# Performance work log

Measured on AMD Instinct MI355X. Metric: run time of the kernel, lower is better.

Reference implementation:

```python
import jax, jax.numpy as jnp
import numpy as np

NUM_NET = 2
V = 100000
D = 128
B = 4096
K = 5
NS = 10
HYP1 = 0.1
HYP2 = 0.1
HYP3 = 0.1


def setup_inputs() -> dict:
    key = jax.random.key(0)
    ks = jax.random.split(key, 10)
    ri = lambda k, shape: jax.random.randint(k, shape, 0, V, dtype=jnp.int32)
    return {
        "node_tables": jax.random.normal(ks[0], (NUM_NET, V, D), jnp.float32) * 0.1,
        "neigh_tables": jax.random.normal(ks[1], (NUM_NET, V, D), jnp.float32) * 0.1,
        "nodes_idx": ri(ks[2], (NUM_NET, B)),
        "neigh_idx": ri(ks[3], (NUM_NET, B, K)),
        "role_idx": ri(ks[4], (NUM_NET, NUM_NET, B)),
        "neg_main": ri(ks[5], (NUM_NET, B, K * NS)),
        "neg_node": ri(ks[6], (NUM_NET, NUM_NET, B, 1 * NS)),
        "neg_cross": ri(ks[7], (NUM_NET, NUM_NET, B, K * NS)),
        "neg_role": ri(ks[8], (NUM_NET, NUM_NET, B, 1 * NS)),
    }


def _pos_loss(ctx, node):
    # ctx: (B, M, D), node: (B, D) -> mean over all logsigmoid(ctx . node)
    return jax.nn.log_sigmoid(jnp.einsum("bmd,bd->bm", ctx, node)).mean()


def _neg_loss(neg_ctx, node):
    # ctx embeddings are negated: logsigmoid(-(neg . node)), sum over samples, mean over batch
    return jax.nn.log_sigmoid(-jnp.einsum("bmd,bd->bm", neg_ctx, node)).sum(axis=1).mean()


def reference(node_tables, neigh_tables, nodes_idx, neigh_idx, role_idx,
              neg_main, neg_node, neg_cross, neg_role):
    cost = []
    for i in range(NUM_NET):
        node_emb = node_tables[i][nodes_idx[i]]          # (B, D)
        # main SGNS loss on view i (neigh tables)
        neigh_emb = neigh_tables[i][neigh_idx[i]]        # (B, K, D)
        c = _pos_loss(neigh_emb, node_emb) + _neg_loss(neigh_tables[i][neg_main[i]], node_emb)
        cost.append(c)
        # cross-view node alignment (node tables of j at same node indices)
        for j in range(NUM_NET):
            if j != i:
                ctx = node_tables[j][nodes_idx[i]][:, None, :]   # (B, 1, D)
                c = _pos_loss(ctx, node_emb) + _neg_loss(node_tables[j][neg_node[i, j]], node_emb)
                cost.append(HYP1 * c)
        # cross-view neighbor loss (neigh tables of j at view-i neighbor indices)
        for j in range(NUM_NET):
            if j != i:
                ctx = neigh_tables[j][neigh_idx[i]]              # (B, K, D)
                c = _pos_loss(ctx, node_emb) + _neg_loss(neigh_tables[j][neg_cross[i, j]], node_emb)
                cost.append(HYP2 * c)
        # role-based loss (node tables of all j at role indices)
        for j in range(NUM_NET):
            ctx = node_tables[j][role_idx[i, j]][:, None, :]     # (B, 1, D)
            c = _pos_loss(ctx, node_emb) + _neg_loss(node_tables[j][neg_role[i, j]], node_emb)
            cost.append(HYP3 * c)
    total = cost[0]
    for c in cost[1:]:
        total = total + c
    return -total / len(cost)
```

## Files before the change

### kernel.cpp

```cpp
#include <hip/hip_runtime.h>

#define NUM_NET 2
#define V 100000
#define D 128
#define B 4096
#define K 5
#define NS 10

#define W_MAIN_POS (1.0f/20480.0f)
#define W_INV_B    (1.0f/4096.0f)
#define HYP_B      (0.1f/4096.0f)
#define HYP2_BK    (0.1f/20480.0f)

#define NBINS 64

__global__ __launch_bounds__(256) void rmne_main(
    const float* __restrict__ node_tables,
    const float* __restrict__ neigh_tables,
    const int*   __restrict__ nodes_idx,
    const int*   __restrict__ neigh_idx,
    const int*   __restrict__ role_idx,
    const int*   __restrict__ neg_main,
    const int*   __restrict__ neg_node,
    const int*   __restrict__ neg_cross,
    const int*   __restrict__ neg_role,
    float*       __restrict__ ws)
{
    const int tid  = threadIdx.x;
    const int lane = tid & 63;
    const int wave = tid >> 6;
    const int unit = blockIdx.x * 4 + wave;
    const int i = unit >> 12;
    const int b = unit & (B - 1);
    const int j = 1 - i;

    int   pk[3];
    float wv[3];
    #pragma unroll
    for (int s = 0; s < 3; ++s) {
        int d = lane + 64 * s;
        int idx = 0; float w = 0.0f; int tab = 0;
        if      (d <   5) { idx = neigh_idx[(i*B + b)*K + d];              w =  W_MAIN_POS; tab = 2 + i; }
        else if (d <  55) { idx = neg_main[(i*B + b)*50 + (d-5)];          w = -W_INV_B;    tab = 2 + i; }
        else if (d <  56) { idx = nodes_idx[i*B + b];                      w =  HYP_B;      tab = j;     }
        else if (d <  66) { idx = neg_node[((i*2+j)*B + b)*NS + (d-56)];   w = -HYP_B;      tab = j;     }
        else if (d <  71) { idx = neigh_idx[(i*B + b)*K + (d-66)];         w =  HYP2_BK;    tab = 2 + j; }
        else if (d < 121) { idx = neg_cross[((i*2+j)*B + b)*50 + (d-71)];  w = -HYP_B;      tab = 2 + j; }
        else if (d < 122) { idx = role_idx[(i*2+0)*B + b];                 w =  HYP_B;      tab = 0;     }
        else if (d < 132) { idx = neg_role[((i*2+0)*B + b)*NS + (d-122)];  w = -HYP_B;      tab = 0;     }
        else if (d < 133) { idx = role_idx[(i*2+1)*B + b];                 w =  HYP_B;      tab = 1;     }
        else if (d < 143) { idx = neg_role[((i*2+1)*B + b)*NS + (d-133)];  w = -HYP_B;      tab = 1;     }
        pk[s] = idx | (tab << 20);
        wv[s] = w;
    }

    const int l16     = lane & 15;
    const int quarter = lane >> 4;
    const int nrow    = nodes_idx[i*B + b];
    const float4* nep = (const float4*)(node_tables + ((size_t)i*V + (size_t)nrow)*D) + l16*2;
    const float4 ne0 = nep[0];
    const float4 ne1 = nep[1];

    float acc = 0.0f;

    auto do_iter = [&](int t, int pks, float wvs) {
        int   src = (4*t + quarter) & 63;
        int   p   = __shfl(pks, src, 64);
        float w   = __shfl(wvs, src, 64);
        int idx = p & 0xFFFFF;
        int tab = p >> 20;
        const float* base = (tab & 2) ? neigh_tables : node_tables;
        const float4* row = (const float4*)(base + ((size_t)(tab & 1)*V + (size_t)idx)*D) + l16*2;
        float4 c0 = row[0];
        float4 c1 = row[1];
        float pp = ne0.x*c0.x + ne0.y*c0.y + ne0.z*c0.z + ne0.w*c0.w
                 + ne1.x*c1.x + ne1.y*c1.y + ne1.z*c1.z + ne1.w*c1.w;
        pp += __shfl_xor(pp, 1, 64);
        pp += __shfl_xor(pp, 2, 64);
        pp += __shfl_xor(pp, 4, 64);
        pp += __shfl_xor(pp, 8, 64);
        float x  = (w < 0.0f) ? -pp : pp;
        float ls = fminf(x, 0.0f) - __logf(1.0f + __expf(-fabsf(x)));
        acc += fabsf(w) * ls;
    };

    #pragma unroll 4
    for (int t = 0;  t < 16; ++t) do_iter(t, pk[0], wv[0]);
    #pragma unroll 4
    for (int t = 16; t < 32; ++t) do_iter(t, pk[1], wv[1]);
    #pragma unroll
    for (int t = 32; t < 36; ++t) do_iter(t, pk[2], wv[2]);

    acc += __shfl_xor(acc, 16, 64);
    acc += __shfl_xor(acc, 32, 64);

    __shared__ float wsum[4];
    if (lane == 0) wsum[wave] = acc;
    __syncthreads();
    if (tid == 0) {
        float s = wsum[0] + wsum[1] + wsum[2] + wsum[3];
        atomicAdd(ws + (blockIdx.x & (NBINS - 1)), s);
    }
}

__global__ void rmne_finalize(const float* __restrict__ ws, float* __restrict__ out)
{
    float v = ws[threadIdx.x];
    v += __shfl_xor(v, 1, 64);
    v += __shfl_xor(v, 2, 64);
    v += __shfl_xor(v, 4, 64);
    v += __shfl_xor(v, 8, 64);
    v += __shfl_xor(v, 16, 64);
    v += __shfl_xor(v, 32, 64);
    if (threadIdx.x == 0) out[0] = v * (-1.0f / 10.0f);
}

extern "C" void kernel_launch(void* const* d_in, const int* in_sizes, int n_in,
                              void* d_out, int out_size, void* d_ws, size_t ws_size,
                              hipStream_t stream) {
    const float* node_tables  = (const float*)d_in[0];
    const float* neigh_tables = (const float*)d_in[1];
    const int*   nodes_idx    = (const int*)d_in[2];
    const int*   neigh_idx    = (const int*)d_in[3];
    const int*   role_idx     = (const int*)d_in[4];
    const int*   neg_main     = (const int*)d_in[5];
    const int*   neg_node     = (const int*)d_in[6];
    const int*   neg_cross    = (const int*)d_in[7];
    const int*   neg_role     = (const int*)d_in[8];
    float* ws  = (float*)d_ws;
    float* out = (float*)d_out;

    hipMemsetAsync(ws, 0, NBINS * sizeof(float), stream);
    rmne_main<<<2048, 256, 0, stream>>>(node_tables, neigh_tables, nodes_idx, neigh_idx,
                                        role_idx, neg_main, neg_node, neg_cross, neg_role, ws);
    rmne_finalize<<<1, 64, 0, stream>>>(ws, out);
}
```

Measured before the change: 261.5 us.

## Assign 4 lanes per row with 8 loads each and drop finalize kernel

Each wavefront now gathers 16 context rows at once with 4 lanes per row, each lane issuing 8 float4 loads, instead of 16 lanes per row with 2 loads. All 9 rounds are fully unrolled so many gathers can be in flight per lane, and the dot-product reduction needs only two shuffles. Per-block sums now go into the output with a single global atomic, which removes the binned workspace and the separate finalize kernel launch. The cost is higher register pressure from 8 float4 loads per lane, capped by launch_bounds(256,4), and atomic contention on one address from 2048 blocks.

```diff
diff --git a/kernel.cpp b/kernel.cpp
--- a/kernel.cpp
+++ b/kernel.cpp
@@ -12,9 +12,7 @@
 #define HYP_B      (0.1f/4096.0f)
 #define HYP2_BK    (0.1f/20480.0f)
 
-#define NBINS 64
-
-__global__ __launch_bounds__(256) void rmne_main(
+__global__ __launch_bounds__(256, 4) void rmne_main(
     const float* __restrict__ node_tables,
     const float* __restrict__ neigh_tables,
     const int*   __restrict__ nodes_idx,
@@ -24,7 +22,7 @@
     const int*   __restrict__ neg_node,
     const int*   __restrict__ neg_cross,
     const int*   __restrict__ neg_role,
-    float*       __restrict__ ws)
+    float*       __restrict__ out)
 {
     const int tid  = threadIdx.x;
     const int lane = tid & 63;
@@ -54,43 +52,49 @@
         wv[s] = w;
     }
 
-    const int l16     = lane & 15;
-    const int quarter = lane >> 4;
-    const int nrow    = nodes_idx[i*B + b];
-    const float4* nep = (const float4*)(node_tables + ((size_t)i*V + (size_t)nrow)*D) + l16*2;
-    const float4 ne0 = nep[0];
-    const float4 ne1 = nep[1];
+    const int lane4 = lane & 3;
+    const int group = lane >> 2;
+
+    int   qi[9];
+    float qw[9];
+    #pragma unroll
+    for (int t = 0; t < 9; ++t) {
+        int src = ((t & 3) << 4) + group;
+        qi[t] = __shfl(pk[t >> 2], src, 64);
+        qw[t] = __shfl(wv[t >> 2], src, 64);
+    }
+
+    const int nrow = nodes_idx[i*B + b];
+    const float4* nrp = (const float4*)(node_tables + ((size_t)i*V + (size_t)nrow)*D);
+    float4 nf[8];
+    #pragma unroll
+    for (int k = 0; k < 8; ++k) nf[k] = nrp[k*4 + lane4];
 
     float acc = 0.0f;
-
-    auto do_iter = [&](int t, int pks, float wvs) {
-        int   src = (4*t + quarter) & 63;
-        int   p   = __shfl(pks, src, 64);
-        float w   = __shfl(wvs, src, 64);
-        int idx = p & 0xFFFFF;
-        int tab = p >> 20;
+    #pragma unroll
+    for (int t = 0; t < 9; ++t) {
+        const int   p   = qi[t];
+        const float w   = qw[t];
+        const int   idx = p & 0xFFFFF;
+        const int   tab = p >> 20;
         const float* base = (tab & 2) ? neigh_tables : node_tables;
-        const float4* row = (const float4*)(base + ((size_t)(tab & 1)*V + (size_t)idx)*D) + l16*2;
-        float4 c0 = row[0];
-        float4 c1 = row[1];
-        float pp = ne0.x*c0.x + ne0.y*c0.y + ne0.z*c0.z + ne0.w*c0.w
-                 + ne1.x*c1.x + ne1.y*c1.y + ne1.z*c1.z + ne1.w*c1.w;
+        const float4* row = (const float4*)(base + ((size_t)(tab & 1)*V + (size_t)idx)*D);
+        float4 c[8];
+        #pragma unroll
+        for (int k = 0; k < 8; ++k) c[k] = row[k*4 + lane4];
+        float pp = 0.0f;
+        #pragma unroll
+        for (int k = 0; k < 8; ++k)
+            pp += nf[k].x*c[k].x + nf[k].y*c[k].y + nf[k].z*c[k].z + nf[k].w*c[k].w;
         pp += __shfl_xor(pp, 1, 64);
         pp += __shfl_xor(pp, 2, 64);
-        pp += __shfl_xor(pp, 4, 64);
-        pp += __shfl_xor(pp, 8, 64);
         float x  = (w < 0.0f) ? -pp : pp;
         float ls = fminf(x, 0.0f) - __logf(1.0f + __expf(-fabsf(x)));
         acc += fabsf(w) * ls;
-    };
+    }
 
-    #pragma unroll 4
-    for (int t = 0;  t < 16; ++t) do_iter(t, pk[0], wv[0]);
-    #pragma unroll 4
-    for (int t = 16; t < 32; ++t) do_iter(t, pk[1], wv[1]);
-    #pragma unroll
-    for (int t = 32; t < 36; ++t) do_iter(t, pk[2], wv[2]);
-
+    acc += __shfl_xor(acc, 4, 64);
+    acc += __shfl_xor(acc, 8, 64);
     acc += __shfl_xor(acc, 16, 64);
     acc += __shfl_xor(acc, 32, 64);
 
@@ -99,20 +103,8 @@
     __syncthreads();
     if (tid == 0) {
         float s = wsum[0] + wsum[1] + wsum[2] + wsum[3];
-        atomicAdd(ws + (blockIdx.x & (NBINS - 1)), s);
+        atomicAdd(out, s * (-1.0f / 10.0f));
     }
-}
-
-__global__ void rmne_finalize(const float* __restrict__ ws, float* __restrict__ out)
-{
-    float v = ws[threadIdx.x];
-    v += __shfl_xor(v, 1, 64);
-    v += __shfl_xor(v, 2, 64);
-    v += __shfl_xor(v, 4, 64);
-    v += __shfl_xor(v, 8, 64);
-    v += __shfl_xor(v, 16, 64);
-    v += __shfl_xor(v, 32, 64);
-    if (threadIdx.x == 0) out[0] = v * (-1.0f / 10.0f);
 }
 
 extern "C" void kernel_launch(void* const* d_in, const int* in_sizes, int n_in,
@@ -127,11 +119,9 @@
     const int*   neg_node     = (const int*)d_in[6];
     const int*   neg_cross    = (const int*)d_in[7];
     const int*   neg_role     = (const int*)d_in[8];
-    float* ws  = (float*)d_ws;
     float* out = (float*)d_out;
 
-    hipMemsetAsync(ws, 0, NBINS * sizeof(float), stream);
+    hipMemsetAsync(out, 0, sizeof(float), stream);
     rmne_main<<<2048, 256, 0, stream>>>(node_tables, neigh_tables, nodes_idx, neigh_idx,
-                                        role_idx, neg_main, neg_node, neg_cross, neg_role, ws);
-    rmne_finalize<<<1, 64, 0, stream>>>(ws, out);
+                                        role_idx, neg_main, neg_node, neg_cross, neg_role, out);
 }
```

Measured after the change: 284.4 us. 8.8% more time.

## Software-pipeline row gathers two deep and drop finalize kernel

Applied to the files above, without the earlier changes.

Restructures the gather loop into a three-stage software pipeline so the embedding row for iteration t+2 is loaded while t is computed. The weight sign and magnitude are now encoded as a 3-bit code packed into the index word, which removes one shuffle per iteration. The separate finalize kernel and binned workspace are removed, and every block atomically adds its scaled partial sum straight into the output. Launch bounds now request 8 waves occupancy. The pipeline costs extra registers, and 2048 atomics on a single address may contend.

```diff
diff --git a/kernel.cpp b/kernel.cpp
--- a/kernel.cpp
+++ b/kernel.cpp
@@ -12,9 +12,8 @@
 #define HYP_B      (0.1f/4096.0f)
 #define HYP2_BK    (0.1f/20480.0f)
 
-#define NBINS 64
 
-__global__ __launch_bounds__(256) void rmne_main(
+__global__ __launch_bounds__(256, 8) void rmne_main(
     const float* __restrict__ node_tables,
     const float* __restrict__ neigh_tables,
     const int*   __restrict__ nodes_idx,
@@ -24,7 +23,7 @@
     const int*   __restrict__ neg_node,
     const int*   __restrict__ neg_cross,
     const int*   __restrict__ neg_role,
-    float*       __restrict__ ws)
+    float*       __restrict__ out)
 {
     const int tid  = threadIdx.x;
     const int lane = tid & 63;
@@ -34,62 +33,90 @@
     const int b = unit & (B - 1);
     const int j = 1 - i;
 
-    int   pk[3];
-    float wv[3];
+    int pk[3];
     #pragma unroll
     for (int s = 0; s < 3; ++s) {
         int d = lane + 64 * s;
-        int idx = 0; float w = 0.0f; int tab = 0;
-        if      (d <   5) { idx = neigh_idx[(i*B + b)*K + d];              w =  W_MAIN_POS; tab = 2 + i; }
-        else if (d <  55) { idx = neg_main[(i*B + b)*50 + (d-5)];          w = -W_INV_B;    tab = 2 + i; }
-        else if (d <  56) { idx = nodes_idx[i*B + b];                      w =  HYP_B;      tab = j;     }
-        else if (d <  66) { idx = neg_node[((i*2+j)*B + b)*NS + (d-56)];   w = -HYP_B;      tab = j;     }
-        else if (d <  71) { idx = neigh_idx[(i*B + b)*K + (d-66)];         w =  HYP2_BK;    tab = 2 + j; }
-        else if (d < 121) { idx = neg_cross[((i*2+j)*B + b)*50 + (d-71)];  w = -HYP_B;      tab = 2 + j; }
-        else if (d < 122) { idx = role_idx[(i*2+0)*B + b];                 w =  HYP_B;      tab = 0;     }
-        else if (d < 132) { idx = neg_role[((i*2+0)*B + b)*NS + (d-122)];  w = -HYP_B;      tab = 0;     }
-        else if (d < 133) { idx = role_idx[(i*2+1)*B + b];                 w =  HYP_B;      tab = 1;     }
-        else if (d < 143) { idx = neg_role[((i*2+1)*B + b)*NS + (d-133)];  w = -HYP_B;      tab = 1;     }
-        pk[s] = idx | (tab << 20);
-        wv[s] = w;
+        int idx = 0, tab = 0, code = 7;
+        if      (d <   5) { idx = neigh_idx[(i*B + b)*K + d];              tab = 2 + i; code = 0; }
+        else if (d <  55) { idx = neg_main[(i*B + b)*50 + (d-5)];          tab = 2 + i; code = 3; }
+        else if (d <  56) { idx = nodes_idx[i*B + b];                      tab = j;     code = 4; }
+        else if (d <  66) { idx = neg_node[((i*2+j)*B + b)*NS + (d-56)];   tab = j;     code = 5; }
+        else if (d <  71) { idx = neigh_idx[(i*B + b)*K + (d-66)];         tab = 2 + j; code = 6; }
+        else if (d < 121) { idx = neg_cross[((i*2+j)*B + b)*50 + (d-71)];  tab = 2 + j; code = 5; }
+        else if (d < 122) { idx = role_idx[(i*2+0)*B + b];                 tab = 0;     code = 4; }
+        else if (d < 132) { idx = neg_role[((i*2+0)*B + b)*NS + (d-122)];  tab = 0;     code = 5; }
+        else if (d < 133) { idx = role_idx[(i*2+1)*B + b];                 tab = 1;     code = 4; }
+        else if (d < 143) { idx = neg_role[((i*2+1)*B + b)*NS + (d-133)];  tab = 1;     code = 5; }
+        pk[s] = idx | (tab << 20) | (code << 22);
     }
 
     const int l16     = lane & 15;
     const int quarter = lane >> 4;
     const int nrow    = nodes_idx[i*B + b];
-    const float4* nep = (const float4*)(node_tables + ((size_t)i*V + (size_t)nrow)*D) + l16*2;
-    const float4 ne0 = nep[0];
-    const float4 ne1 = nep[1];
+    const float4* nrp = (const float4*)(node_tables + ((size_t)i*V + (size_t)nrow)*D) + l16*2;
+    const float4 ne0 = nrp[0];
+    const float4 ne1 = nrp[1];
 
     float acc = 0.0f;
 
-    auto do_iter = [&](int t, int pks, float wvs) {
-        int   src = (4*t + quarter) & 63;
-        int   p   = __shfl(pks, src, 64);
-        float w   = __shfl(wvs, src, 64);
-        int idx = p & 0xFFFFF;
-        int tab = p >> 20;
+    int e_cur, e_mid, e_nxt;
+    float4 cc0, cc1, m0, m1, n0, n1;
+
+    auto rowload = [&](int e, float4& r0, float4& r1) {
+        int idx = e & 0xFFFFF;
+        int tab = (e >> 20) & 3;
         const float* base = (tab & 2) ? neigh_tables : node_tables;
         const float4* row = (const float4*)(base + ((size_t)(tab & 1)*V + (size_t)idx)*D) + l16*2;
-        float4 c0 = row[0];
-        float4 c1 = row[1];
-        float pp = ne0.x*c0.x + ne0.y*c0.y + ne0.z*c0.z + ne0.w*c0.w
-                 + ne1.x*c1.x + ne1.y*c1.y + ne1.z*c1.z + ne1.w*c1.w;
+        r0 = row[0];
+        r1 = row[1];
+    };
+
+    auto compute = [&]() {
+        float pp = ne0.x*cc0.x + ne0.y*cc0.y + ne0.z*cc0.z + ne0.w*cc0.w
+                 + ne1.x*cc1.x + ne1.y*cc1.y + ne1.z*cc1.z + ne1.w*cc1.w;
         pp += __shfl_xor(pp, 1, 64);
         pp += __shfl_xor(pp, 2, 64);
         pp += __shfl_xor(pp, 4, 64);
         pp += __shfl_xor(pp, 8, 64);
-        float x  = (w < 0.0f) ? -pp : pp;
+        int code = (e_cur >> 22) & 7;
+        float mag = (code == 0) ? W_MAIN_POS
+                  : (code == 3) ? W_INV_B
+                  : (code == 6) ? HYP2_BK
+                  : (code == 7) ? 0.0f
+                  : HYP_B;
+        float x  = (code & 1) ? -pp : pp;
         float ls = fminf(x, 0.0f) - __logf(1.0f + __expf(-fabsf(x)));
-        acc += fabsf(w) * ls;
+        acc += mag * ls;
+    };
+
+    auto rotate = [&]() {
+        e_cur = e_mid; cc0 = m0; cc1 = m1;
+        e_mid = e_nxt; m0  = n0; m1  = n1;
+    };
+
+    e_cur = __shfl(pk[0], quarter, 64);
+    rowload(e_cur, cc0, cc1);
+    e_mid = __shfl(pk[0], 4 + quarter, 64);
+    rowload(e_mid, m0, m1);
+
+    auto step = [&](int tn, int slotpk) {
+        e_nxt = __shfl(slotpk, (4*tn + quarter) & 63, 64);
+        rowload(e_nxt, n0, n1);
+        compute();
+        rotate();
     };
 
     #pragma unroll 4
-    for (int t = 0;  t < 16; ++t) do_iter(t, pk[0], wv[0]);
+    for (int tn = 2;  tn < 16; ++tn) step(tn, pk[0]);
     #pragma unroll 4
-    for (int t = 16; t < 32; ++t) do_iter(t, pk[1], wv[1]);
+    for (int tn = 16; tn < 32; ++tn) step(tn, pk[1]);
     #pragma unroll
-    for (int t = 32; t < 36; ++t) do_iter(t, pk[2], wv[2]);
+    for (int tn = 32; tn < 36; ++tn) step(tn, pk[2]);
+
+    compute();
+    e_cur = e_mid; cc0 = m0; cc1 = m1;
+    compute();
 
     acc += __shfl_xor(acc, 16, 64);
     acc += __shfl_xor(acc, 32, 64);
@@ -99,20 +126,8 @@
     __syncthreads();
     if (tid == 0) {
         float s = wsum[0] + wsum[1] + wsum[2] + wsum[3];
-        atomicAdd(ws + (blockIdx.x & (NBINS - 1)), s);
+        atomicAdd(out, s * (-1.0f / 10.0f));
     }
-}
-
-__global__ void rmne_finalize(const float* __restrict__ ws, float* __restrict__ out)
-{
-    float v = ws[threadIdx.x];
-    v += __shfl_xor(v, 1, 64);
-    v += __shfl_xor(v, 2, 64);
-    v += __shfl_xor(v, 4, 64);
-    v += __shfl_xor(v, 8, 64);
-    v += __shfl_xor(v, 16, 64);
-    v += __shfl_xor(v, 32, 64);
-    if (threadIdx.x == 0) out[0] = v * (-1.0f / 10.0f);
 }
 
 extern "C" void kernel_launch(void* const* d_in, const int* in_sizes, int n_in,
@@ -127,11 +142,9 @@
     const int*   neg_node     = (const int*)d_in[6];
     const int*   neg_cross    = (const int*)d_in[7];
     const int*   neg_role     = (const int*)d_in[8];
-    float* ws  = (float*)d_ws;
     float* out = (float*)d_out;
 
-    hipMemsetAsync(ws, 0, NBINS * sizeof(float), stream);
+    hipMemsetAsync(out, 0, sizeof(float), stream);
     rmne_main<<<2048, 256, 0, stream>>>(node_tables, neigh_tables, nodes_idx, neigh_idx,
-                                        role_idx, neg_main, neg_node, neg_cross, neg_role, ws);
-    rmne_finalize<<<1, 64, 0, stream>>>(ws, out);
+                                        role_idx, neg_main, neg_node, neg_cross, neg_role, out);
 }
```

Measured after the change: 285.6 us. +9.2%, slower.

## Invert gather into per-row bucketed scatter and stream table rows once

Applied to the files above, without the earlier changes.

Replaces the per-unit random gather of about 1.2M table rows with a three-stage scheme. It first copies the node embeddings into a compact buffer, then atomically buckets every (unit, code) reference by destination table row, then sweeps all 400k rows so that each referenced row is read once and dotted against the compact node embeddings. The goal is to turn scattered row reads into a linear sweep. The cost is extra launches, hundreds of thousands of global atomics, a multi-MB workspace memset, and a sweep over all rows including unreferenced ones. The old gather kernel is kept as a fallback when the workspace is too small, and the final reduction now uses one atomic directly on the output.

```diff
diff --git a/kernel.cpp b/kernel.cpp
--- a/kernel.cpp
+++ b/kernel.cpp
@@ -7,14 +7,178 @@
 #define K 5
 #define NS 10
 
+#define NROWS  400000
+#define NUNITS 8192
+#define NENT   144
+#define SLOTS  12
+#define OVF_CAP 16384
+
 #define W_MAIN_POS (1.0f/20480.0f)
 #define W_INV_B    (1.0f/4096.0f)
 #define HYP_B      (0.1f/4096.0f)
 #define HYP2_BK    (0.1f/20480.0f)
 
-#define NBINS 64
-
-__global__ __launch_bounds__(256) void rmne_main(
+#define WS_COUNTS 0
+#define WS_CURSOR 400000
+#define WS_U      400064
+#define WS_SLOTS  1448640
+#define WS_OVF    6248640
+#define WS_NEEDED ((size_t)(6281408) * 4)
+
+__device__ __forceinline__ float dot8(float4 a0, float4 a1, float4 b0, float4 b1) {
+    return a0.x*b0.x + a0.y*b0.y + a0.z*b0.z + a0.w*b0.w
+         + a1.x*b1.x + a1.y*b1.y + a1.z*b1.z + a1.w*b1.w;
+}
+
+__device__ __forceinline__ float wlogsig(float pp, int code) {
+    float mag = (code == 0) ? W_MAIN_POS
+              : (code == 3) ? W_INV_B
+              : (code == 6) ? HYP2_BK
+              : (code == 7) ? 0.0f
+              : HYP_B;
+    float x  = (code & 1) ? -pp : pp;
+    float ls = fminf(x, 0.0f) - __logf(1.0f + __expf(-fabsf(x)));
+    return mag * ls;
+}
+
+__global__ __launch_bounds__(256) void rmne_build_u(
+    const float* __restrict__ node_tables,
+    const int*   __restrict__ nodes_idx,
+    float*       __restrict__ ws)
+{
+    float4* U4 = (float4*)(ws + WS_U);
+    int t = blockIdx.x * 256 + threadIdx.x;
+    int u = t >> 5;
+    int k = t & 31;
+    int i = u >> 12;
+    int nrow = nodes_idx[u];
+    const float4* src = (const float4*)(node_tables + ((size_t)i*V + (size_t)nrow)*D);
+    U4[(size_t)u*32 + k] = src[k];
+}
+
+__global__ __launch_bounds__(256) void rmne_scatter(
+    const int* __restrict__ nodes_idx,
+    const int* __restrict__ neigh_idx,
+    const int* __restrict__ role_idx,
+    const int* __restrict__ neg_main,
+    const int* __restrict__ neg_node,
+    const int* __restrict__ neg_cross,
+    const int* __restrict__ neg_role,
+    int*       __restrict__ ws_i)
+{
+    int* counts = ws_i + WS_COUNTS;
+    int* cursor = ws_i + WS_CURSOR;
+    int* slots  = ws_i + WS_SLOTS;
+    int* ovf    = ws_i + WS_OVF;
+
+    int gid = blockIdx.x * 256 + threadIdx.x;
+    int u = gid / NENT;
+    int e = gid - u * NENT;
+    int i = u >> 12;
+    int b = u & (B - 1);
+    int j = 1 - i;
+
+    int idx, tab, code;
+    if      (e <   5) { idx = neigh_idx[(i*B + b)*K + e];              tab = 2 + i; code = 0; }
+    else if (e <  55) { idx = neg_main[(i*B + b)*50 + (e-5)];          tab = 2 + i; code = 3; }
+    else if (e <  56) { idx = nodes_idx[i*B + b];                      tab = j;     code = 4; }
+    else if (e <  66) { idx = neg_node[((i*2+j)*B + b)*NS + (e-56)];   tab = j;     code = 5; }
+    else if (e <  71) { idx = neigh_idx[(i*B + b)*K + (e-66)];         tab = 2 + j; code = 6; }
+    else if (e < 121) { idx = neg_cross[((i*2+j)*B + b)*50 + (e-71)];  tab = 2 + j; code = 5; }
+    else if (e < 122) { idx = role_idx[(i*2+0)*B + b];                 tab = 0;     code = 4; }
+    else if (e < 132) { idx = neg_role[((i*2+0)*B + b)*NS + (e-122)];  tab = 0;     code = 5; }
+    else if (e < 133) { idx = role_idx[(i*2+1)*B + b];                 tab = 1;     code = 4; }
+    else if (e < 143) { idx = neg_role[((i*2+1)*B + b)*NS + (e-133)];  tab = 1;     code = 5; }
+    else return;
+
+    int g = tab * V + idx;
+    int pack = u | (code << 13);
+    int s = atomicAdd(&counts[g], 1);
+    if (s < SLOTS) {
+        slots[(size_t)g * SLOTS + s] = pack;
+    } else {
+        int o = atomicAdd(cursor, 1);
+        if (o < OVF_CAP) { ovf[2*o] = g; ovf[2*o + 1] = pack; }
+    }
+}
+
+__global__ __launch_bounds__(256) void rmne_stream(
+    const float* __restrict__ node_tables,
+    const float* __restrict__ neigh_tables,
+    const float* __restrict__ ws,
+    float*       __restrict__ out)
+{
+    const int* ws_i   = (const int*)ws;
+    const int* counts = ws_i + WS_COUNTS;
+    const int* slots  = ws_i + WS_SLOTS;
+    const int* ovf    = ws_i + WS_OVF;
+    const float* U    = ws + WS_U;
+
+    const int tid     = threadIdx.x;
+    const int lane    = tid & 63;
+    const int wave    = tid >> 6;
+    const int l16     = lane & 15;
+    const int quarter = lane >> 4;
+    const int qid     = (blockIdx.x * 4 + wave) * 4 + quarter;
+    const int QTOT    = 2048 * 16;
+
+    float acc = 0.0f;
+
+    for (int g = qid; g < NROWS; g += QTOT) {
+        int c = counts[g];
+        if (c == 0) continue;
+        const float* rowb = (g < 2*V) ? node_tables + (size_t)g * D
+                                      : neigh_tables + (size_t)(g - 2*V) * D;
+        const float4* row = (const float4*)rowb + l16*2;
+        float4 r0 = row[0];
+        float4 r1 = row[1];
+        int cc = (c < SLOTS) ? c : SLOTS;
+        for (int s = 0; s < cc; ++s) {
+            int p = slots[(size_t)g * SLOTS + s];
+            int u = p & (NUNITS - 1);
+            int code = p >> 13;
+            const float4* up = (const float4*)(U + (size_t)u * D) + l16*2;
+            float pp = dot8(r0, r1, up[0], up[1]);
+            pp += __shfl_xor(pp, 1, 64);
+            pp += __shfl_xor(pp, 2, 64);
+            pp += __shfl_xor(pp, 4, 64);
+            pp += __shfl_xor(pp, 8, 64);
+            acc += wlogsig(pp, code);
+        }
+    }
+
+    int n_ovf = ws_i[WS_CURSOR];
+    if (n_ovf > OVF_CAP) n_ovf = OVF_CAP;
+    for (int o = qid; o < n_ovf; o += QTOT) {
+        int g = ovf[2*o];
+        int p = ovf[2*o + 1];
+        int u = p & (NUNITS - 1);
+        int code = p >> 13;
+        const float* rowb = (g < 2*V) ? node_tables + (size_t)g * D
+                                      : neigh_tables + (size_t)(g - 2*V) * D;
+        const float4* row = (const float4*)rowb + l16*2;
+        const float4* up  = (const float4*)(U + (size_t)u * D) + l16*2;
+        float pp = dot8(row[0], row[1], up[0], up[1]);
+        pp += __shfl_xor(pp, 1, 64);
+        pp += __shfl_xor(pp, 2, 64);
+        pp += __shfl_xor(pp, 4, 64);
+        pp += __shfl_xor(pp, 8, 64);
+        acc += wlogsig(pp, code);
+    }
+
+    acc += __shfl_xor(acc, 16, 64);
+    acc += __shfl_xor(acc, 32, 64);
+
+    __shared__ float wsum[4];
+    if (lane == 0) wsum[wave] = acc;
+    __syncthreads();
+    if (tid == 0) {
+        float s = wsum[0] + wsum[1] + wsum[2] + wsum[3];
+        atomicAdd(out, s * (-1.0f / 10.0f));
+    }
+}
+
+__global__ __launch_bounds__(256) void rmne_gather(
     const float* __restrict__ node_tables,
     const float* __restrict__ neigh_tables,
     const int*   __restrict__ nodes_idx,
@@ -24,7 +188,7 @@
     const int*   __restrict__ neg_node,
     const int*   __restrict__ neg_cross,
     const int*   __restrict__ neg_role,
-    float*       __restrict__ ws)
+    float*       __restrict__ out)
 {
     const int tid  = threadIdx.x;
     const int lane = tid & 63;
@@ -73,8 +237,7 @@
         const float4* row = (const float4*)(base + ((size_t)(tab & 1)*V + (size_t)idx)*D) + l16*2;
         float4 c0 = row[0];
         float4 c1 = row[1];
-        float pp = ne0.x*c0.x + ne0.y*c0.y + ne0.z*c0.z + ne0.w*c0.w
-                 + ne1.x*c1.x + ne1.y*c1.y + ne1.z*c1.z + ne1.w*c1.w;
+        float pp = dot8(ne0, ne1, c0, c1);
         pp += __shfl_xor(pp, 1, 64);
         pp += __shfl_xor(pp, 2, 64);
         pp += __shfl_xor(pp, 4, 64);
@@ -99,20 +262,8 @@
     __syncthreads();
     if (tid == 0) {
         float s = wsum[0] + wsum[1] + wsum[2] + wsum[3];
-        atomicAdd(ws + (blockIdx.x & (NBINS - 1)), s);
-    }
-}
-
-__global__ void rmne_finalize(const float* __restrict__ ws, float* __restrict__ out)
-{
-    float v = ws[threadIdx.x];
-    v += __shfl_xor(v, 1, 64);
-    v += __shfl_xor(v, 2, 64);
-    v += __shfl_xor(v, 4, 64);
-    v += __shfl_xor(v, 8, 64);
-    v += __shfl_xor(v, 16, 64);
-    v += __shfl_xor(v, 32, 64);
-    if (threadIdx.x == 0) out[0] = v * (-1.0f / 10.0f);
+        atomicAdd(out, s * (-1.0f / 10.0f));
+    }
 }
 
 extern "C" void kernel_launch(void* const* d_in, const int* in_sizes, int n_in,
@@ -127,11 +278,20 @@
     const int*   neg_node     = (const int*)d_in[6];
     const int*   neg_cross    = (const int*)d_in[7];
     const int*   neg_role     = (const int*)d_in[8];
-    float* ws  = (float*)d_ws;
     float* out = (float*)d_out;
 
-    hipMemsetAsync(ws, 0, NBINS * sizeof(float), stream);
-    rmne_main<<<2048, 256, 0, stream>>>(node_tables, neigh_tables, nodes_idx, neigh_idx,
-                                        role_idx, neg_main, neg_node, neg_cross, neg_role, ws);
-    rmne_finalize<<<1, 64, 0, stream>>>(ws, out);
-}
+    hipMemsetAsync(out, 0, sizeof(float), stream);
+
+    if (ws_size >= WS_NEEDED) {
+        float* ws = (float*)d_ws;
+        hipMemsetAsync(d_ws, 0, (size_t)(WS_U) * 4, stream);
+        rmne_build_u<<<1024, 256, 0, stream>>>(node_tables, nodes_idx, ws);
+        rmne_scatter<<<4608, 256, 0, stream>>>(nodes_idx, neigh_idx, role_idx,
+                                               neg_main, neg_node, neg_cross, neg_role,
+                                               (int*)d_ws);
+        rmne_stream<<<2048, 256, 0, stream>>>(node_tables, neigh_tables, ws, out);
+    } else {
+        rmne_gather<<<2048, 256, 0, stream>>>(node_tables, neigh_tables, nodes_idx, neigh_idx,
+                                              role_idx, neg_main, neg_node, neg_cross, neg_role, out);
+    }
+}
```

After: 381.6 us. 1.46x slower.
